# Optimization experiments

Measured on AMD Instinct MI355X. Metric: run time of the kernel, lower is better.

## Reference

```python
import jax, jax.numpy as jnp
import numpy as np

B, S, D, H, L = 2, 4096, 768, 12, 12
DH = D // H
BS = 16                # block size
NB = S // BS           # 256 blocks
NR = 2                 # random blocks per middle query block
DFF = 3072
VOCAB = 50358


def layer_norm(x, s, b):
    m = x.mean(-1, keepdims=True)
    v = ((x - m) ** 2).mean(-1, keepdims=True)
    return (x - m) * jax.lax.rsqrt(v + 1e-12) * s + b


def setup_inputs() -> dict:
    key = jax.random.key(0)
    ks = jax.random.split(key, 20)
    rn = lambda k, shp: jax.random.normal(k, shp, jnp.float32) * 0.02
    # random key-block indices per middle query block, avoiding window+global blocks
    rng = np.random.default_rng(0)
    rb = np.zeros((NB - 2, NR), np.int32)
    for i in range(1, NB - 1):
        forbidden = {0, i - 1, i, i + 1, NB - 1}
        choices = np.array([b for b in range(NB) if b not in forbidden])
        rb[i - 1] = rng.choice(choices, NR, replace=False)
    return {
        "input_ids": jax.random.randint(ks[0], (B, S), 0, VOCAB, jnp.int32),
        "rand_blocks": jnp.asarray(rb),
        "emb_word": rn(ks[1], (VOCAB, D)),
        "emb_pos": rn(ks[2], (S, D)),
        "ln0_s": jnp.ones((D,)), "ln0_b": jnp.zeros((D,)),
        "Wq": rn(ks[3], (L, D, D)), "bq": jnp.zeros((L, D)),
        "Wk": rn(ks[4], (L, D, D)), "bk": jnp.zeros((L, D)),
        "Wv": rn(ks[5], (L, D, D)), "bv": jnp.zeros((L, D)),
        "Wo": rn(ks[6], (L, D, D)), "bo": jnp.zeros((L, D)),
        "ln1_s": jnp.ones((L, D)), "ln1_b": jnp.zeros((L, D)),
        "W1": rn(ks[7], (L, D, DFF)), "b1": jnp.zeros((L, DFF)),
        "W2": rn(ks[8], (L, DFF, D)), "b2": jnp.zeros((L, D)),
        "ln2_s": jnp.ones((L, D)), "ln2_b": jnp.zeros((L, D)),
        "Wp": rn(ks[9], (D, D)), "bp": jnp.zeros((D,)),
        "start_w": jax.random.normal(ks[10], (D,), jnp.float32),
        "end_w": jax.random.normal(ks[11], (D,), jnp.float32),
        "Wd1": rn(ks[12], (D, 20)), "bd1": jnp.zeros((20,)),
        "Wd2": rn(ks[13], (20, 2)), "bd2": jnp.zeros((2,)),
    }


def block_sparse_attn(h, wq, bq_, wk, bk_, wv, bv_, wo, bo_, rand_blocks):
    scale = 1.0 / np.sqrt(DH)
    heads = lambda w, b: (h @ w + b).reshape(B, S, H, DH).transpose(0, 2, 1, 3)
    q = heads(wq, bq_) * scale
    k = heads(wk, bk_)
    v = heads(wv, bv_)
    qb = q.reshape(B, H, NB, BS, DH)
    kb = k.reshape(B, H, NB, BS, DH)
    vb = v.reshape(B, H, NB, BS, DH)
    # global query blocks (first & last) attend to every key
    qg = qb[:, :, jnp.array([0, NB - 1])]                       # [B,H,2,BS,DH]
    ag = jax.nn.softmax(jnp.einsum('bhgqd,bhkd->bhgqk', qg, k), -1)
    og = jnp.einsum('bhgqk,bhkd->bhgqd', ag, v)
    # middle query blocks: global(2) + window(3) + random(2) key blocks
    mid = jnp.arange(1, NB - 1, dtype=jnp.int32)
    idx = jnp.concatenate([
        jnp.zeros((NB - 2, 1), jnp.int32),
        jnp.full((NB - 2, 1), NB - 1, jnp.int32),
        jnp.stack([mid - 1, mid, mid + 1], -1),
        rand_blocks.astype(jnp.int32),
    ], axis=1)                                                  # [NB-2, 7]
    kg = kb[:, :, idx].reshape(B, H, NB - 2, 7 * BS, DH)        # gathered keys
    vg = vb[:, :, idx].reshape(B, H, NB - 2, 7 * BS, DH)
    qm = qb[:, :, 1:NB - 1]                                     # [B,H,NB-2,BS,DH]
    am = jax.nn.softmax(jnp.einsum('bhnqd,bhnkd->bhnqk', qm, kg), -1)
    om = jnp.einsum('bhnqk,bhnkd->bhnqd', am, vg)
    ob = jnp.concatenate([og[:, :, :1], om, og[:, :, 1:]], axis=2)  # [B,H,NB,BS,DH]
    o = ob.reshape(B, H, S, DH).transpose(0, 2, 1, 3).reshape(B, S, D)
    return o @ wo + bo_


def encoder(input_ids, rand_blocks, emb_word, emb_pos, ln0_s, ln0_b,
            Wq, bq, Wk, bk, Wv, bv, Wo, bo, ln1_s, ln1_b,
            W1, b1, W2, b2, ln2_s, ln2_b):
    h = layer_norm(emb_word[input_ids] + emb_pos[None], ln0_s, ln0_b)

    def layer(hc, p):
        wq, bq_, wk, bk_, wv, bv_, wo, bo_, l1s, l1b, w1, b1_, w2, b2_, l2s, l2b = p
        a = block_sparse_attn(hc, wq, bq_, wk, bk_, wv, bv_, wo, bo_, rand_blocks)
        hc = layer_norm(hc + a, l1s, l1b)
        f = jax.nn.gelu(hc @ w1 + b1_, approximate=False) @ w2 + b2_
        hc = layer_norm(hc + f, l2s, l2b)
        return hc, None

    h, _ = jax.lax.scan(layer, h, (Wq, bq, Wk, bk, Wv, bv, Wo, bo,
                                   ln1_s, ln1_b, W1, b1, W2, b2, ln2_s, ln2_b))
    return h


def reference(input_ids, rand_blocks, emb_word, emb_pos, ln0_s, ln0_b,
              Wq, bq, Wk, bk, Wv, bv, Wo, bo, ln1_s, ln1_b,
              W1, b1, W2, b2, ln2_s, ln2_b, Wp, bp,
              start_w, end_w, Wd1, bd1, Wd2, bd2):
    h = encoder(input_ids, rand_blocks, emb_word, emb_pos, ln0_s, ln0_b,
                Wq, bq, Wk, bk, Wv, bv, Wo, bo, ln1_s, ln1_b,
                W1, b1, W2, b2, ln2_s, ln2_b)
    start_logits = h @ start_w        # [B,S]
    end_logits = h @ end_w            # [B,S]
    pooled = jnp.tanh(h[:, 0] @ Wp + bp)   # BERT-style pooler on [CLS]
    d1 = jax.nn.relu(pooled @ Wd1 + bd1)
    disc_logits = d1 @ Wd2 + bd2      # [B,2]
    return start_logits, end_logits, disc_logits
```

## Files before the change

kernel.cpp:

```cpp
#include <hip/hip_runtime.h>

#define DEV __device__ __forceinline__

typedef unsigned short u16;
typedef short bf16x8 __attribute__((ext_vector_type(8)));
typedef float f32x4 __attribute__((ext_vector_type(4)));

constexpr int Bc = 2, Sc = 4096, Dc = 768, Hc = 12, Lc = 12;
constexpr int BSc = 16, NBc = 256, NRc = 2, DFFc = 3072;
constexpr int Mr = Bc * Sc;

DEV u16 f2b(float f) {
  unsigned u = __builtin_bit_cast(unsigned, f);
  u += 0x7fffu + ((u >> 16) & 1u);
  return (u16)(u >> 16);
}
DEV float b2f(u16 u) { return __builtin_bit_cast(float, (unsigned)u << 16); }

DEV void gload_lds16(const void* g, void* l) {
  __builtin_amdgcn_global_load_lds((const __attribute__((address_space(1))) void*)g,
                                   (__attribute__((address_space(3))) void*)l, 16, 0, 0);
}

template<int EPI>
__global__ __launch_bounds__(512, 1)
void gemmP(const u16* __restrict__ A, const u16* __restrict__ Bt,
           const float* __restrict__ bias, u16* __restrict__ Cb,
           u16* __restrict__ Qh, u16* __restrict__ Kh,
           u16* __restrict__ VhT, int M, int N, int K)
{
  __shared__ u16 As[2][128 * 64];
  __shared__ u16 Bs[2][256 * 64];
  const int tid = threadIdx.x;
  const int wid = tid >> 6, lane = tid & 63;
  const int fr = lane & 15, fq = lane >> 4;
  const int wr = wid >> 2, wc = wid & 3;

  int nwg = gridDim.x * gridDim.y;
  int orig = blockIdx.y * gridDim.x + blockIdx.x;
  int swz = (nwg & 7) ? orig : (orig & 7) * (nwg >> 3) + (orig >> 3);
  int bx = swz % gridDim.x, by = swz / gridDim.x;
  const int m0 = by * 128, n0 = bx * 256;

  const u16* asrc[2];
  const u16* bsrc[4];
#pragma unroll
  for (int p = 0; p < 2; ++p) {
    int ci = p * 512 + tid;
    int r = ci >> 3, c = (ci & 7) ^ (r & 7);
    asrc[p] = A + (size_t)(m0 + r) * K + c * 8;
  }
#pragma unroll
  for (int p = 0; p < 4; ++p) {
    int ci = p * 512 + tid;
    int r = ci >> 3, c = (ci & 7) ^ (r & 7);
    bsrc[p] = Bt + (size_t)(n0 + r) * K + c * 8;
  }
  auto stageA = [&](int buf, int k0) {
#pragma unroll
    for (int p = 0; p < 2; ++p)
      gload_lds16(asrc[p] + k0, &As[buf][(p * 512 + tid) * 8]);
  };
  auto stageB = [&](int buf, int k0) {
#pragma unroll
    for (int p = 0; p < 4; ++p)
      gload_lds16(bsrc[p] + k0, &Bs[buf][(p * 512 + tid) * 8]);
  };

  f32x4 acc[4][4] = {};
  const int arow = wr * 64 + fr;
  const int brow = wc * 64 + fr;

  stageA(0, 0);  stageB(0, 0);
  stageA(1, 64); stageB(1, 64);
  asm volatile("s_waitcnt vmcnt(6)" ::: "memory");
  __builtin_amdgcn_sched_barrier(0);
  __builtin_amdgcn_s_barrier();

  const int nt = K >> 6;
  for (int kt = 0; kt < nt; ++kt) {
    const u16* ab = As[kt & 1];
    const u16* bb = Bs[kt & 1];
    bf16x8 aA[2][2], aB[2][2], bA[2][2], bB[2][2];

#pragma unroll
    for (int f = 0; f < 2; ++f)
#pragma unroll
      for (int kh = 0; kh < 2; ++kh) {
        int rowa = arow + f * 16;
        aA[f][kh] = *(const bf16x8*)(ab + rowa * 64 + (((kh * 4 + fq) ^ (rowa & 7)) << 3));
        int rowb = brow + f * 16;
        bA[f][kh] = *(const bf16x8*)(bb + rowb * 64 + (((kh * 4 + fq) ^ (rowb & 7)) << 3));
      }
    __builtin_amdgcn_s_setprio(1);
#pragma unroll
    for (int m = 0; m < 2; ++m)
#pragma unroll
      for (int n = 0; n < 2; ++n)
#pragma unroll
        for (int kh = 0; kh < 2; ++kh)
          acc[m][n] = __builtin_amdgcn_mfma_f32_16x16x32_bf16(aA[m][kh], bA[n][kh], acc[m][n], 0, 0, 0);
    __builtin_amdgcn_s_setprio(0);

#pragma unroll
    for (int f = 0; f < 2; ++f)
#pragma unroll
      for (int kh = 0; kh < 2; ++kh) {
        int rowb = brow + 32 + f * 16;
        bB[f][kh] = *(const bf16x8*)(bb + rowb * 64 + (((kh * 4 + fq) ^ (rowb & 7)) << 3));
      }
    __builtin_amdgcn_s_setprio(1);
#pragma unroll
    for (int m = 0; m < 2; ++m)
#pragma unroll
      for (int n = 0; n < 2; ++n)
#pragma unroll
        for (int kh = 0; kh < 2; ++kh)
          acc[m][n + 2] = __builtin_amdgcn_mfma_f32_16x16x32_bf16(aA[m][kh], bB[n][kh], acc[m][n + 2], 0, 0, 0);
    __builtin_amdgcn_s_setprio(0);
    asm volatile("s_waitcnt lgkmcnt(0)" ::: "memory");
    __builtin_amdgcn_sched_barrier(0);
    __builtin_amdgcn_s_barrier();

    if (kt + 2 < nt) stageB(kt & 1, (kt + 2) * 64);
#pragma unroll
    for (int f = 0; f < 2; ++f)
#pragma unroll
      for (int kh = 0; kh < 2; ++kh) {
        int rowa = arow + 32 + f * 16;
        aB[f][kh] = *(const bf16x8*)(ab + rowa * 64 + (((kh * 4 + fq) ^ (rowa & 7)) << 3));
      }
    __builtin_amdgcn_s_setprio(1);
#pragma unroll
    for (int m = 0; m < 2; ++m)
#pragma unroll
      for (int n = 0; n < 2; ++n)
#pragma unroll
        for (int kh = 0; kh < 2; ++kh)
          acc[m + 2][n] = __builtin_amdgcn_mfma_f32_16x16x32_bf16(aB[m][kh], bA[n][kh], acc[m + 2][n], 0, 0, 0);
    __builtin_amdgcn_s_setprio(0);
    asm volatile("s_waitcnt lgkmcnt(0)" ::: "memory");
    __builtin_amdgcn_sched_barrier(0);
    __builtin_amdgcn_s_barrier();

    if (kt + 2 < nt) stageA(kt & 1, (kt + 2) * 64);
    __builtin_amdgcn_s_setprio(1);
#pragma unroll
    for (int m = 0; m < 2; ++m)
#pragma unroll
      for (int n = 0; n < 2; ++n)
#pragma unroll
        for (int kh = 0; kh < 2; ++kh)
          acc[m + 2][n + 2] = __builtin_amdgcn_mfma_f32_16x16x32_bf16(aB[m][kh], bB[n][kh], acc[m + 2][n + 2], 0, 0, 0);
    __builtin_amdgcn_s_setprio(0);
    if (kt + 1 < nt) {
      if (kt + 2 < nt) asm volatile("s_waitcnt vmcnt(6)" ::: "memory");
      else             asm volatile("s_waitcnt vmcnt(0)" ::: "memory");
      __builtin_amdgcn_sched_barrier(0);
      __builtin_amdgcn_s_barrier();
    }
  }

#pragma unroll
  for (int m = 0; m < 4; ++m) {
#pragma unroll
    for (int n = 0; n < 4; ++n) {
      int col = n0 + wc * 64 + n * 16 + fr;
      float bv = bias[col];
      if constexpr (EPI == 2) {
        int sec = col / 768;
        int c = col - sec * 768;
        int hh = c >> 6, dd = c & 63;
#pragma unroll
        for (int r = 0; r < 4; ++r) {
          int row = m0 + wr * 64 + m * 16 + fq * 4 + r;
          int bb2 = row >> 12, ss = row & 4095;
          size_t bhh = (size_t)(bb2 * Hc + hh);
          u16 val = f2b(acc[m][n][r] + bv);
          if (sec == 0) Qh[(bhh * Sc + ss) * 64 + dd] = val;
          else if (sec == 1) Kh[(bhh * Sc + ss) * 64 + dd] = val;
          else VhT[(bhh * 64 + dd) * Sc + ss] = val;
        }
      } else {
#pragma unroll
        for (int r = 0; r < 4; ++r) {
          int row = m0 + wr * 64 + m * 16 + fq * 4 + r;
          float v = acc[m][n][r] + bv;
          v = 0.5f * v * (1.f + erff(v * 0.70710678118654752f));
          Cb[(size_t)row * N + col] = f2b(v);
        }
      }
    }
  }
}

__global__ __launch_bounds__(256, 2)
void gemmQ(const u16* __restrict__ A, const u16* __restrict__ Bt,
           const float* __restrict__ bias, u16* __restrict__ Cb,
           int M, int N, int K)
{
  __shared__ u16 As[2][128 * 64];
  __shared__ u16 Bs[2][128 * 64];
  const int tid = threadIdx.x;
  const int wid = tid >> 6, lane = tid & 63;
  const int fr = lane & 15, fq = lane >> 4;
  const int wr = wid >> 1, wc = wid & 1;

  int nwg = gridDim.x * gridDim.y;
  int orig = blockIdx.y * gridDim.x + blockIdx.x;
  int swz = (nwg & 7) ? orig : (orig & 7) * (nwg >> 3) + (orig >> 3);
  int bx = swz % gridDim.x, by = swz / gridDim.x;
  const int m0 = by * 128, n0 = bx * 128;

  const u16* asrc[4];
  const u16* bsrc[4];
#pragma unroll
  for (int p = 0; p < 4; ++p) {
    int ci = p * 256 + tid;
    int r = ci >> 3, c = (ci & 7) ^ (r & 7);
    asrc[p] = A + (size_t)(m0 + r) * K + c * 8;
    bsrc[p] = Bt + (size_t)(n0 + r) * K + c * 8;
  }
  auto stageA = [&](int buf, int k0) {
#pragma unroll
    for (int p = 0; p < 4; ++p)
      gload_lds16(asrc[p] + k0, &As[buf][(p * 256 + tid) * 8]);
  };
  auto stageB = [&](int buf, int k0) {
#pragma unroll
    for (int p = 0; p < 4; ++p)
      gload_lds16(bsrc[p] + k0, &Bs[buf][(p * 256 + tid) * 8]);
  };

  f32x4 acc[4][4] = {};
  const int arow = wr * 64 + fr;
  const int brow = wc * 64 + fr;

  stageA(0, 0);  stageB(0, 0);
  stageA(1, 64); stageB(1, 64);
  asm volatile("s_waitcnt vmcnt(8)" ::: "memory");
  __builtin_amdgcn_sched_barrier(0);
  __builtin_amdgcn_s_barrier();

  const int nt = K >> 6;
  for (int kt = 0; kt < nt; ++kt) {
    const u16* ab = As[kt & 1];
    const u16* bb = Bs[kt & 1];
    bf16x8 aA[2][2], aB[2][2], bA[2][2], bB[2][2];

#pragma unroll
    for (int f = 0; f < 2; ++f)
#pragma unroll
      for (int kh = 0; kh < 2; ++kh) {
        int rowa = arow + f * 16;
        aA[f][kh] = *(const bf16x8*)(ab + rowa * 64 + (((kh * 4 + fq) ^ (rowa & 7)) << 3));
        int rowb = brow + f * 16;
        bA[f][kh] = *(const bf16x8*)(bb + rowb * 64 + (((kh * 4 + fq) ^ (rowb & 7)) << 3));
      }
    __builtin_amdgcn_s_setprio(1);
#pragma unroll
    for (int m = 0; m < 2; ++m)
#pragma unroll
      for (int n = 0; n < 2; ++n)
#pragma unroll
        for (int kh = 0; kh < 2; ++kh)
          acc[m][n] = __builtin_amdgcn_mfma_f32_16x16x32_bf16(aA[m][kh], bA[n][kh], acc[m][n], 0, 0, 0);
    __builtin_amdgcn_s_setprio(0);

#pragma unroll
    for (int f = 0; f < 2; ++f)
#pragma unroll
      for (int kh = 0; kh < 2; ++kh) {
        int rowb = brow + 32 + f * 16;
        bB[f][kh] = *(const bf16x8*)(bb + rowb * 64 + (((kh * 4 + fq) ^ (rowb & 7)) << 3));
      }
    __builtin_amdgcn_s_setprio(1);
#pragma unroll
    for (int m = 0; m < 2; ++m)
#pragma unroll
      for (int n = 0; n < 2; ++n)
#pragma unroll
        for (int kh = 0; kh < 2; ++kh)
          acc[m][n + 2] = __builtin_amdgcn_mfma_f32_16x16x32_bf16(aA[m][kh], bB[n][kh], acc[m][n + 2], 0, 0, 0);
    __builtin_amdgcn_s_setprio(0);
    asm volatile("s_waitcnt lgkmcnt(0)" ::: "memory");
    __builtin_amdgcn_sched_barrier(0);
    __builtin_amdgcn_s_barrier();

    if (kt + 2 < nt) stageB(kt & 1, (kt + 2) * 64);
#pragma unroll
    for (int f = 0; f < 2; ++f)
#pragma unroll
      for (int kh = 0; kh < 2; ++kh) {
        int rowa = arow + 32 + f * 16;
        aB[f][kh] = *(const bf16x8*)(ab + rowa * 64 + (((kh * 4 + fq) ^ (rowa & 7)) << 3));
      }
    __builtin_amdgcn_s_setprio(1);
#pragma unroll
    for (int m = 0; m < 2; ++m)
#pragma unroll
      for (int n = 0; n < 2; ++n)
#pragma unroll
        for (int kh = 0; kh < 2; ++kh)
          acc[m + 2][n] = __builtin_amdgcn_mfma_f32_16x16x32_bf16(aB[m][kh], bA[n][kh], acc[m + 2][n], 0, 0, 0);
    __builtin_amdgcn_s_setprio(0);
    asm volatile("s_waitcnt lgkmcnt(0)" ::: "memory");
    __builtin_amdgcn_sched_barrier(0);
    __builtin_amdgcn_s_barrier();

    if (kt + 2 < nt) stageA(kt & 1, (kt + 2) * 64);
    __builtin_amdgcn_s_setprio(1);
#pragma unroll
    for (int m = 0; m < 2; ++m)
#pragma unroll
      for (int n = 0; n < 2; ++n)
#pragma unroll
        for (int kh = 0; kh < 2; ++kh)
          acc[m + 2][n + 2] = __builtin_amdgcn_mfma_f32_16x16x32_bf16(aB[m][kh], bB[n][kh], acc[m + 2][n + 2], 0, 0, 0);
    __builtin_amdgcn_s_setprio(0);
    if (kt + 1 < nt) {
      if (kt + 2 < nt) asm volatile("s_waitcnt vmcnt(8)" ::: "memory");
      else             asm volatile("s_waitcnt vmcnt(0)" ::: "memory");
      __builtin_amdgcn_sched_barrier(0);
      __builtin_amdgcn_s_barrier();
    }
  }

#pragma unroll
  for (int m = 0; m < 4; ++m) {
#pragma unroll
    for (int n = 0; n < 4; ++n) {
      int col = n0 + wc * 64 + n * 16 + fr;
      float bv = bias[col];
#pragma unroll
      for (int r = 0; r < 4; ++r) {
        int row = m0 + wr * 64 + m * 16 + fq * 4 + r;
        Cb[(size_t)row * N + col] = f2b(acc[m][n][r] + bv);
      }
    }
  }
}

__global__ __launch_bounds__(256)
void wtrans_all(const float* __restrict__ Wq, const float* __restrict__ Wk,
                const float* __restrict__ Wv, const float* __restrict__ Wo,
                const float* __restrict__ W1, const float* __restrict__ W2,
                u16* __restrict__ wqkvT, u16* __restrict__ woT,
                u16* __restrict__ w1T, u16* __restrict__ w2T)
{
  int bx = blockIdx.x;
  size_t l = blockIdx.y;
  size_t wsq = l * 768 * 768, wff = l * 768 * 3072;
  const float* in; u16* out; int K, N, ntx, t; float scale = 1.f;
  if (bx < 144)       { in = Wq + wsq; out = wqkvT + l * 2304 * 768;           K = 768;  N = 768;  ntx = 12; t = bx;        scale = 0.125f; }
  else if (bx < 288)  { in = Wk + wsq; out = wqkvT + l * 2304 * 768 + 589824;  K = 768;  N = 768;  ntx = 12; t = bx - 144;  }
  else if (bx < 432)  { in = Wv + wsq; out = wqkvT + l * 2304 * 768 + 1179648; K = 768;  N = 768;  ntx = 12; t = bx - 288;  }
  else if (bx < 576)  { in = Wo + wsq; out = woT + l * 768 * 768;              K = 768;  N = 768;  ntx = 12; t = bx - 432;  }
  else if (bx < 1152) { in = W1 + wff; out = w1T + l * 3072 * 768;             K = 768;  N = 3072; ntx = 48; t = bx - 576;  }
  else                { in = W2 + wff; out = w2T + l * 768 * 3072;             K = 3072; N = 768;  ntx = 12; t = bx - 1152; }
  int n0 = (t % ntx) * 64, k0 = (t / ntx) * 64;
  __shared__ float tl[64][65];
  int tid = threadIdx.x;
  int kr = tid >> 4, nc = (tid & 15) * 4;
#pragma unroll
  for (int kk = 0; kk < 4; ++kk) {
    float4 v = *(const float4*)(in + (size_t)(k0 + kk * 16 + kr) * N + n0 + nc);
    float* d = &tl[kk * 16 + kr][nc];
    d[0] = v.x; d[1] = v.y; d[2] = v.z; d[3] = v.w;
  }
  __syncthreads();
  int k2 = (tid & 31) * 2, nr = tid >> 5;
#pragma unroll
  for (int nn = 0; nn < 8; ++nn) {
    int n = nn * 8 + nr;
    unsigned pk = (unsigned)f2b(tl[k2][n] * scale) | ((unsigned)f2b(tl[k2 + 1][n] * scale) << 16);
    *(unsigned*)(out + (size_t)(n0 + n) * K + k0 + k2) = pk;
  }
}

__global__ void pack_bias(const float* __restrict__ bq, const float* __restrict__ bk,
                          const float* __restrict__ bv, float* __restrict__ bqkv)
{
  int i = blockIdx.x * 256 + threadIdx.x;
  if (i >= Lc * 2304) return;
  int l = i / 2304, j = i % 2304;
  float v = (j < 768) ? bq[(size_t)l * 768 + j] * 0.125f
          : (j < 1536) ? bk[(size_t)l * 768 + j - 768]
                       : bv[(size_t)l * 768 + j - 1536];
  bqkv[i] = v;
}

DEV void breduce2(float& a, float& b) {
  __shared__ float ra[4], rbv[4];
  for (int off = 32; off > 0; off >>= 1) {
    a += __shfl_down(a, off);
    b += __shfl_down(b, off);
  }
  int lane = threadIdx.x & 63, wid = threadIdx.x >> 6;
  if (lane == 0) { ra[wid] = a; rbv[wid] = b; }
  __syncthreads();
  a = ra[0] + ra[1] + ra[2] + ra[3];
  b = rbv[0] + rbv[1] + rbv[2] + rbv[3];
}

__global__ __launch_bounds__(256)
void embed_ln(const int* __restrict__ ids, const float* __restrict__ ew,
              const float* __restrict__ ep, const float* __restrict__ gs,
              const float* __restrict__ gb, float* __restrict__ hout, u16* __restrict__ hb)
{
  int row = blockIdx.x;
  int spos = row & (Sc - 1);
  int id = ids[row];
  int tid = threadIdx.x;
  float x[3], sum = 0.f, ss = 0.f;
#pragma unroll
  for (int j = 0; j < 3; ++j) {
    int i = tid + j * 256;
    x[j] = ew[(size_t)id * Dc + i] + ep[(size_t)spos * Dc + i];
    sum += x[j]; ss += x[j] * x[j];
  }
  breduce2(sum, ss);
  float mean = sum * (1.f / Dc);
  float var = ss * (1.f / Dc) - mean * mean;
  float inv = rsqrtf(var + 1e-12f);
#pragma unroll
  for (int j = 0; j < 3; ++j) {
    int i = tid + j * 256;
    float y = (x[j] - mean) * inv * gs[i] + gb[i];
    hout[(size_t)row * Dc + i] = y;
    hb[(size_t)row * Dc + i] = f2b(y);
  }
}

__global__ __launch_bounds__(256)
void ln_res(const float* __restrict__ X, const u16* __restrict__ Rb,
            const float* __restrict__ gs, const float* __restrict__ gb,
            float* __restrict__ Yf, u16* __restrict__ Yb)
{
  const int wid = threadIdx.x >> 6, lane = threadIdx.x & 63;
  const int row = blockIdx.x * 4 + wid;
  const float* xr = X + (size_t)row * Dc;
  const u16*   rr = Rb + (size_t)row * Dc;
  float x[12];
  float sum = 0.f, ss = 0.f;
#pragma unroll
  for (int p = 0; p < 3; ++p) {
    int c = p * 256 + lane * 4;
    float4 xv = *(const float4*)(xr + c);
    ushort4 rv = *(const ushort4*)(rr + c);
    float v0 = xv.x + b2f(rv.x);
    float v1 = xv.y + b2f(rv.y);
    float v2 = xv.z + b2f(rv.z);
    float v3 = xv.w + b2f(rv.w);
    x[p * 4 + 0] = v0; x[p * 4 + 1] = v1; x[p * 4 + 2] = v2; x[p * 4 + 3] = v3;
    sum += (v0 + v1) + (v2 + v3);
    ss  += (v0 * v0 + v1 * v1) + (v2 * v2 + v3 * v3);
  }
#pragma unroll
  for (int off = 1; off < 64; off <<= 1) {
    sum += __shfl_xor(sum, off);
    ss  += __shfl_xor(ss, off);
  }
  float mean = sum * (1.f / Dc);
  float var = ss * (1.f / Dc) - mean * mean;
  float inv = rsqrtf(var + 1e-12f);
#pragma unroll
  for (int p = 0; p < 3; ++p) {
    int c = p * 256 + lane * 4;
    float4 gv = *(const float4*)(gs + c);
    float4 bv = *(const float4*)(gb + c);
    float y0 = (x[p * 4 + 0] - mean) * inv * gv.x + bv.x;
    float y1 = (x[p * 4 + 1] - mean) * inv * gv.y + bv.y;
    float y2 = (x[p * 4 + 2] - mean) * inv * gv.z + bv.z;
    float y3 = (x[p * 4 + 3] - mean) * inv * gv.w + bv.w;
    float4 yo; yo.x = y0; yo.y = y1; yo.z = y2; yo.w = y3;
    *(float4*)(Yf + (size_t)row * Dc + c) = yo;
    ushort4 pk; pk.x = f2b(y0); pk.y = f2b(y1); pk.z = f2b(y2); pk.w = f2b(y3);
    *(ushort4*)(Yb + (size_t)row * Dc + c) = pk;
  }
}

__global__ __launch_bounds__(256)
void gattn_flash(const u16* __restrict__ Qh, const u16* __restrict__ Kh,
                 const u16* __restrict__ VhT, float* __restrict__ part)
{
  __shared__ u16 pb[4][16 * 136];
  __shared__ float ob[4][16][64];
  __shared__ float mlb[4][2][16];
  const int kc = blockIdx.x, g = blockIdx.y, bh = blockIdx.z;
  const int wid = threadIdx.x >> 6, lane = threadIdx.x & 63;
  const int fr = lane & 15, fq = lane >> 4;
  const int qrow = g ? (NBc - 1) * BSc : 0;

  const u16* Qb = Qh + ((size_t)bh * Sc + qrow) * 64;
  const u16* Kb = Kh + (size_t)bh * Sc * 64;
  const u16* Vt = VhT + (size_t)bh * 64 * Sc;

  bf16x8 qa0 = *(const bf16x8*)(Qb + fr * 64 + fq * 8);
  bf16x8 qa1 = *(const bf16x8*)(Qb + fr * 64 + 32 + fq * 8);

  float m[4], l[4];
  f32x4 o[4] = {};
#pragma unroll
  for (int r = 0; r < 4; ++r) { m[r] = -3.4e38f; l[r] = 0.f; }

  u16* pbw = pb[wid];
  const int s0w = kc * 256 + wid * 64;

  for (int it = 0; it < 2; ++it) {
    const int sb = s0w + it * 32;
    f32x4 s[2];
#pragma unroll
    for (int t = 0; t < 2; ++t) {
      const u16* kr = Kb + (size_t)(sb + t * 16 + fr) * 64 + fq * 8;
      bf16x8 kb0 = *(const bf16x8*)(kr);
      bf16x8 kb1 = *(const bf16x8*)(kr + 32);
      f32x4 a = {};
      a = __builtin_amdgcn_mfma_f32_16x16x32_bf16(qa0, kb0, a, 0, 0, 0);
      a = __builtin_amdgcn_mfma_f32_16x16x32_bf16(qa1, kb1, a, 0, 0, 0);
      s[t] = a;
    }
#pragma unroll
    for (int r = 0; r < 4; ++r) {
      float pm = fmaxf(s[0][r], s[1][r]);
#pragma unroll
      for (int off = 1; off < 16; off <<= 1) pm = fmaxf(pm, __shfl_xor(pm, off));
      float nm = fmaxf(m[r], pm);
      float sc = __expf(m[r] - nm);
      m[r] = nm;
      float e0 = __expf(s[0][r] - nm), e1 = __expf(s[1][r] - nm);
      float ps = e0 + e1;
#pragma unroll
      for (int off = 1; off < 16; off <<= 1) ps += __shfl_xor(ps, off);
      l[r] = l[r] * sc + ps;
#pragma unroll
      for (int nn = 0; nn < 4; ++nn) o[nn][r] *= sc;
      pbw[(fq * 4 + r) * 136 + fr] = f2b(e0);
      pbw[(fq * 4 + r) * 136 + 16 + fr] = f2b(e1);
    }
    asm volatile("s_waitcnt lgkmcnt(0)" ::: "memory");
    __builtin_amdgcn_sched_barrier(0);
    bf16x8 pa = *(const bf16x8*)(pbw + fr * 136 + fq * 8);
#pragma unroll
    for (int nn = 0; nn < 4; ++nn) {
      bf16x8 vb = *(const bf16x8*)(Vt + (size_t)(nn * 16 + fr) * Sc + sb + fq * 8);
      o[nn] = __builtin_amdgcn_mfma_f32_16x16x32_bf16(pa, vb, o[nn], 0, 0, 0);
    }
  }

#pragma unroll
  for (int nn = 0; nn < 4; ++nn)
#pragma unroll
    for (int r = 0; r < 4; ++r)
      ob[wid][fq * 4 + r][nn * 16 + fr] = o[nn][r];
  if (fr == 0) {
#pragma unroll
    for (int r = 0; r < 4; ++r) {
      mlb[wid][0][fq * 4 + r] = m[r];
      mlb[wid][1][fq * 4 + r] = l[r];
    }
  }
  __syncthreads();

  float* pp = part + (size_t)(((bh * 2 + g) * 16) + kc) * 1056;
  int tid = threadIdx.x;
#pragma unroll
  for (int k = 0; k < 4; ++k) {
    int oidx = tid + k * 256;
    int q = oidx >> 6, d = oidx & 63;
    float M = fmaxf(fmaxf(mlb[0][0][q], mlb[1][0][q]), fmaxf(mlb[2][0][q], mlb[3][0][q]));
    float O = 0.f, L = 0.f;
#pragma unroll
    for (int w = 0; w < 4; ++w) {
      float f = __expf(mlb[w][0][q] - M);
      O += f * ob[w][q][d];
      L += f * mlb[w][1][q];
    }
    pp[q * 64 + d] = O;
    if (d == 0) { pp[1024 + q] = M; pp[1040 + q] = L; }
  }
}

__global__ __launch_bounds__(256)
void attn_tail(const u16* __restrict__ Qh, const u16* __restrict__ Kh,
               const u16* __restrict__ VhT, const int* __restrict__ rb,
               const float* __restrict__ part, u16* __restrict__ attnb)
{
  if (blockIdx.x < 48) {
    int idx = blockIdx.x;
    int bh = idx >> 1, g = idx & 1;
    int b = bh / Hc, h = bh % Hc;
    int tid = threadIdx.x;
    const float* pbase = part + (size_t)idx * 16 * 1056;
#pragma unroll
    for (int k = 0; k < 4; ++k) {
      int oidx = tid + k * 256;
      int q = oidx >> 6, d = oidx & 63;
      float M = -3.4e38f;
#pragma unroll
      for (int c = 0; c < 16; ++c) M = fmaxf(M, pbase[c * 1056 + 1024 + q]);
      float O = 0.f, L = 0.f;
#pragma unroll
      for (int c = 0; c < 16; ++c) {
        float f = __expf(pbase[c * 1056 + 1024 + q] - M);
        O += f * pbase[c * 1056 + q * 64 + d];
        L += f * pbase[c * 1056 + 1040 + q];
      }
      int srow = (g ? (NBc - 1) * BSc : 0) + q;
      attnb[((size_t)(b * Sc + srow)) * Dc + h * 64 + d] = f2b(O / L);
    }
    return;
  }

  __shared__ u16 pb[4][16 * 136];
  const int wid = threadIdx.x >> 6, lane = threadIdx.x & 63;
  const int w = (blockIdx.x - 48) * 4 + wid;
  const int n = w % 254, bh = w / 254;
  const int b = bh / Hc, h = bh % Hc;
  const int fr = lane & 15, fq = lane >> 4;

  int idx[7];
  idx[0] = 0; idx[1] = NBc - 1; idx[2] = n; idx[3] = n + 1; idx[4] = n + 2;
  idx[5] = rb[n * NRc]; idx[6] = rb[n * NRc + 1];

  const u16* Qb = Qh + ((size_t)bh * Sc + (n + 1) * BSc) * 64;
  const u16* Kb = Kh + (size_t)bh * Sc * 64;
  const u16* Vt = VhT + (size_t)bh * 64 * Sc;

  bf16x8 qa0 = *(const bf16x8*)(Qb + fr * 64 + fq * 8);
  bf16x8 qa1 = *(const bf16x8*)(Qb + fr * 64 + 32 + fq * 8);

  f32x4 s[7];
#pragma unroll
  for (int t = 0; t < 7; ++t) {
    const u16* kr = Kb + ((size_t)idx[t] * BSc + fr) * 64 + fq * 8;
    bf16x8 kb0 = *(const bf16x8*)(kr);
    bf16x8 kb1 = *(const bf16x8*)(kr + 32);
    f32x4 a = {};
    a = __builtin_amdgcn_mfma_f32_16x16x32_bf16(qa0, kb0, a, 0, 0, 0);
    a = __builtin_amdgcn_mfma_f32_16x16x32_bf16(qa1, kb1, a, 0, 0, 0);
    s[t] = a;
  }

  float mx[4], sm[4];
#pragma unroll
  for (int r = 0; r < 4; ++r) {
    mx[r] = s[0][r];
#pragma unroll
    for (int t = 1; t < 7; ++t) mx[r] = fmaxf(mx[r], s[t][r]);
  }
#pragma unroll
  for (int off = 1; off < 16; off <<= 1)
#pragma unroll
    for (int r = 0; r < 4; ++r) mx[r] = fmaxf(mx[r], __shfl_xor(mx[r], off));
#pragma unroll
  for (int r = 0; r < 4; ++r) sm[r] = 0.f;
#pragma unroll
  for (int t = 0; t < 7; ++t)
#pragma unroll
    for (int r = 0; r < 4; ++r) { float e = expf(s[t][r] - mx[r]); s[t][r] = e; sm[r] += e; }
#pragma unroll
  for (int off = 1; off < 16; off <<= 1)
#pragma unroll
    for (int r = 0; r < 4; ++r) sm[r] += __shfl_xor(sm[r], off);
  float inv[4];
#pragma unroll
  for (int r = 0; r < 4; ++r) inv[r] = 1.f / sm[r];

  u16* pbw = pb[wid];
#pragma unroll
  for (int t = 0; t < 7; ++t)
#pragma unroll
    for (int r = 0; r < 4; ++r)
      pbw[(fq * 4 + r) * 136 + t * 16 + fr] = f2b(s[t][r] * inv[r]);
  for (int i = lane; i < 16 * 24; i += 64) {
    int rr = i / 24, cc = 112 + i % 24;
    pbw[rr * 136 + cc] = 0;
  }
  __syncthreads();

  f32x4 o[4] = {};
#pragma unroll
  for (int ks = 0; ks < 4; ++ks) {
    bf16x8 pa = *(const bf16x8*)(pbw + fr * 136 + ks * 32 + fq * 8);
    int t = ks * 2 + (fq >> 1);
    int tt = (t < 7) ? t : 0;
    size_t voff = (size_t)idx[tt] * BSc + (fq & 1) * 8;
#pragma unroll
    for (int nn = 0; nn < 4; ++nn) {
      bf16x8 vb = *(const bf16x8*)(Vt + (size_t)(nn * 16 + fr) * Sc + voff);
      o[nn] = __builtin_amdgcn_mfma_f32_16x16x32_bf16(pa, vb, o[nn], 0, 0, 0);
    }
  }

  size_t rbase = (size_t)b * Sc + (n + 1) * BSc;
#pragma unroll
  for (int nn = 0; nn < 4; ++nn)
#pragma unroll
    for (int r = 0; r < 4; ++r)
      attnb[(rbase + fq * 4 + r) * Dc + h * 64 + nn * 16 + fr] = f2b(o[nn][r]);
}

__global__ __launch_bounds__(256)
void logits_k(const float* __restrict__ h, const float* __restrict__ sw,
              const float* __restrict__ ew, float* __restrict__ out)
{
  int row = blockIdx.x;
  int tid = threadIdx.x;
  float s1 = 0.f, s2 = 0.f;
#pragma unroll
  for (int j = 0; j < 3; ++j) {
    int i = tid + j * 256;
    float x = h[(size_t)row * Dc + i];
    s1 += x * sw[i]; s2 += x * ew[i];
  }
  breduce2(s1, s2);
  if (tid == 0) { out[row] = s1; out[Mr + row] = s2; }
}

__global__ __launch_bounds__(256)
void pooled_k(const float* __restrict__ h, const float* __restrict__ Wp,
              const float* __restrict__ bp, float* __restrict__ pooled)
{
  int b = blockIdx.y, j0 = blockIdx.x * 64;
  int jl = threadIdx.x & 63, kp = threadIdx.x >> 6;
  __shared__ float hr[768];
  __shared__ float part[4][64];
  for (int i = threadIdx.x; i < 768; i += 256) hr[i] = h[(size_t)b * Sc * Dc + i];
  __syncthreads();
  float a0 = 0.f, a1 = 0.f, a2 = 0.f, a3 = 0.f;
  const float* wp = Wp + (size_t)(kp * 192) * 768 + j0 + jl;
  const float* hk = hr + kp * 192;
#pragma unroll 4
  for (int k = 0; k < 192; k += 4) {
    a0 += hk[k]     * wp[(size_t)k * 768];
    a1 += hk[k + 1] * wp[(size_t)(k + 1) * 768];
    a2 += hk[k + 2] * wp[(size_t)(k + 2) * 768];
    a3 += hk[k + 3] * wp[(size_t)(k + 3) * 768];
  }
  part[kp][jl] = a0 + a1 + a2 + a3;
  __syncthreads();
  if (threadIdx.x < 64) {
    float s = part[0][jl] + part[1][jl] + part[2][jl] + part[3][jl] + bp[j0 + jl];
    pooled[b * 768 + j0 + jl] = tanhf(s);
  }
}

__global__ __launch_bounds__(256)
void head2(const float* __restrict__ pooled, const float* __restrict__ Wd1,
           const float* __restrict__ bd1, const float* __restrict__ Wd2,
           const float* __restrict__ bd2, float* __restrict__ out)
{
  __shared__ float pl[1536];
  __shared__ float part[40][6];
  __shared__ float d1[40];
  int tid = threadIdx.x;
  for (int i = tid; i < 1536; i += 256) pl[i] = pooled[i];
  __syncthreads();
  if (tid < 240) {
    int p = tid / 6, s = tid % 6;
    int b = p / 20, u = p % 20;
    float a = 0.f;
    for (int k = s * 128; k < s * 128 + 128; ++k) a += pl[b * 768 + k] * Wd1[(size_t)k * 20 + u];
    part[p][s] = a;
  }
  __syncthreads();
  if (tid < 40) {
    float a = bd1[tid % 20];
#pragma unroll
    for (int s = 0; s < 6; ++s) a += part[tid][s];
    d1[tid] = fmaxf(a, 0.f);
  }
  __syncthreads();
  if (tid < 4) {
    int b = tid >> 1, o = tid & 1;
    float a = bd2[o];
#pragma unroll
    for (int k = 0; k < 20; ++k) a += d1[b * 20 + k] * Wd2[k * 2 + o];
    out[2 * Mr + b * 2 + o] = a;
  }
}

extern "C" void kernel_launch(void* const* d_in, const int* in_sizes, int n_in,
                              void* d_out, int out_size, void* d_ws, size_t ws_size,
                              hipStream_t stream)
{
  (void)in_sizes; (void)n_in; (void)out_size; (void)ws_size;
  const int*   ids   = (const int*)d_in[0];
  const int*   rbp   = (const int*)d_in[1];
  const float* emb_w = (const float*)d_in[2];
  const float* emb_p = (const float*)d_in[3];
  const float* ln0s  = (const float*)d_in[4];
  const float* ln0b  = (const float*)d_in[5];
  const float* Wq    = (const float*)d_in[6];
  const float* bq    = (const float*)d_in[7];
  const float* Wk    = (const float*)d_in[8];
  const float* bk    = (const float*)d_in[9];
  const float* Wv    = (const float*)d_in[10];
  const float* bv    = (const float*)d_in[11];
  const float* Wo    = (const float*)d_in[12];
  const float* bo    = (const float*)d_in[13];
  const float* ln1s  = (const float*)d_in[14];
  const float* ln1b  = (const float*)d_in[15];
  const float* W1    = (const float*)d_in[16];
  const float* b1    = (const float*)d_in[17];
  const float* W2    = (const float*)d_in[18];
  const float* b2    = (const float*)d_in[19];
  const float* ln2s  = (const float*)d_in[20];
  const float* ln2b  = (const float*)d_in[21];
  const float* Wp    = (const float*)d_in[22];
  const float* bp    = (const float*)d_in[23];
  const float* sw    = (const float*)d_in[24];
  const float* ewv   = (const float*)d_in[25];
  const float* Wd1   = (const float*)d_in[26];
  const float* bd1   = (const float*)d_in[27];
  const float* Wd2   = (const float*)d_in[28];
  const float* bd2   = (const float*)d_in[29];
  float* out = (float*)d_out;

  unsigned char* pc = (unsigned char*)d_ws;
  auto carve = [&](size_t bytes) {
    void* r = (void*)pc;
    pc += (bytes + 255) & ~(size_t)255;
    return r;
  };
  u16*   wqkvT = (u16*)carve((size_t)Lc * 2304 * 768 * 2);
  u16*   woT   = (u16*)carve((size_t)Lc * 768 * 768 * 2);
  u16*   w1T   = (u16*)carve((size_t)Lc * 3072 * 768 * 2);
  u16*   w2T   = (u16*)carve((size_t)Lc * 768 * 3072 * 2);
  float* bqkv  = (float*)carve((size_t)Lc * 2304 * 4);
  float* h     = (float*)carve((size_t)Mr * Dc * 4);
  u16*   hb    = (u16*)carve((size_t)Mr * Dc * 2);
  u16*   Qh    = (u16*)carve((size_t)Mr * Dc * 2);
  u16*   Kh    = (u16*)carve((size_t)Mr * Dc * 2);
  u16*   VhT   = (u16*)carve((size_t)Mr * Dc * 2);
  u16*   attnb = (u16*)carve((size_t)Mr * Dc * 2);
  u16*   c0b   = (u16*)carve((size_t)Mr * Dc * 2);
  float* pool2 = (float*)carve((size_t)Bc * Dc * 4);
  float* m1ws  = (float*)carve((size_t)Mr * DFFc * 2);
  u16*   m1    = (u16*)m1ws;
  float* part  = (float*)((unsigned char*)m1ws + (size_t)13 * 1024 * 1024);

  pack_bias<<<(Lc * 2304 + 255) / 256, 256, 0, stream>>>(bq, bk, bv, bqkv);
  wtrans_all<<<dim3(1728, Lc), 256, 0, stream>>>(Wq, Wk, Wv, Wo, W1, W2,
                                                 wqkvT, woT, w1T, w2T);
  embed_ln<<<Mr, 256, 0, stream>>>(ids, emb_w, emb_p, ln0s, ln0b, h, hb);

  for (int l = 0; l < Lc; ++l) {
    gemmP<2><<<dim3(9, 64), 512, 0, stream>>>(hb, wqkvT + (size_t)l * 2304 * 768,
                                              bqkv + (size_t)l * 2304,
                                              nullptr, Qh, Kh, VhT, Mr, 2304, 768);
    gattn_flash<<<dim3(16, 2, Bc * Hc), 256, 0, stream>>>(Qh, Kh, VhT, part);
    attn_tail<<<48 + 1524, 256, 0, stream>>>(Qh, Kh, VhT, rbp, part, attnb);
    gemmQ<<<dim3(6, 64), 256, 0, stream>>>(attnb, woT + (size_t)l * 768 * 768,
                                           bo + (size_t)l * 768, c0b, Mr, 768, 768);
    ln_res<<<Mr / 4, 256, 0, stream>>>(h, c0b, ln1s + (size_t)l * 768, ln1b + (size_t)l * 768, h, hb);
    gemmP<1><<<dim3(12, 64), 512, 0, stream>>>(hb, w1T + (size_t)l * 3072 * 768,
                                               b1 + (size_t)l * 3072,
                                               m1, nullptr, nullptr, nullptr,
                                               Mr, 3072, 768);
    gemmQ<<<dim3(6, 64), 256, 0, stream>>>(m1, w2T + (size_t)l * 768 * 3072,
                                           b2 + (size_t)l * 768, c0b, Mr, 768, 3072);
    ln_res<<<Mr / 4, 256, 0, stream>>>(h, c0b, ln2s + (size_t)l * 768, ln2b + (size_t)l * 768, h, hb);
  }

  logits_k<<<Mr, 256, 0, stream>>>(h, sw, ewv, out);
  pooled_k<<<dim3(12, Bc), 256, 0, stream>>>(h, Wp, bp, pool2);
  head2<<<1, 256, 0, stream>>>(pool2, Wd1, bd1, Wd2, bd2, out);
}
```

Measured before the change: 3.582 ms.

## Merge global flash attention with middle-block attention, split out small reduce

Global-query flash partial blocks and sliding/random middle-block attention now run in one launch, and the global partial reduction moves into a small separate kernel. This lets the 768 global blocks overlap with the 1524 middle blocks instead of serialising two launches, leaving only a tiny 48-block reduce afterwards. Separately, the weight-transpose kernel writes 16-byte packed stores instead of 4-byte stores. Launch count is unchanged, and the reduce kernel adds a small serial tail.

```diff
diff --git a/kernel.cpp b/kernel.cpp
--- a/kernel.cpp
+++ b/kernel.cpp
@@ -369,12 +369,16 @@
     d[0] = v.x; d[1] = v.y; d[2] = v.z; d[3] = v.w;
   }
   __syncthreads();
-  int k2 = (tid & 31) * 2, nr = tid >> 5;
-#pragma unroll
-  for (int nn = 0; nn < 8; ++nn) {
-    int n = nn * 8 + nr;
-    unsigned pk = (unsigned)f2b(tl[k2][n] * scale) | ((unsigned)f2b(tl[k2 + 1][n] * scale) << 16);
-    *(unsigned*)(out + (size_t)(n0 + n) * K + k0 + k2) = pk;
+  int k8 = (tid & 7) * 8, nb = tid >> 3;
+#pragma unroll
+  for (int half = 0; half < 2; ++half) {
+    int n = nb + half * 32;
+    unsigned pk0 = (unsigned)f2b(tl[k8 + 0][n] * scale) | ((unsigned)f2b(tl[k8 + 1][n] * scale) << 16);
+    unsigned pk1 = (unsigned)f2b(tl[k8 + 2][n] * scale) | ((unsigned)f2b(tl[k8 + 3][n] * scale) << 16);
+    unsigned pk2 = (unsigned)f2b(tl[k8 + 4][n] * scale) | ((unsigned)f2b(tl[k8 + 5][n] * scale) << 16);
+    unsigned pk3 = (unsigned)f2b(tl[k8 + 6][n] * scale) | ((unsigned)f2b(tl[k8 + 7][n] * scale) << 16);
+    uint4 pk; pk.x = pk0; pk.y = pk1; pk.z = pk2; pk.w = pk3;
+    *(uint4*)(out + (size_t)(n0 + n) * K + k0 + k8) = pk;
   }
 }
 
@@ -481,143 +485,114 @@
 }
 
 __global__ __launch_bounds__(256)
-void gattn_flash(const u16* __restrict__ Qh, const u16* __restrict__ Kh,
-                 const u16* __restrict__ VhT, float* __restrict__ part)
+void gattn_fm(const u16* __restrict__ Qh, const u16* __restrict__ Kh,
+              const u16* __restrict__ VhT, const int* __restrict__ rb,
+              float* __restrict__ part, u16* __restrict__ attnb)
 {
   __shared__ u16 pb[4][16 * 136];
   __shared__ float ob[4][16][64];
   __shared__ float mlb[4][2][16];
-  const int kc = blockIdx.x, g = blockIdx.y, bh = blockIdx.z;
   const int wid = threadIdx.x >> 6, lane = threadIdx.x & 63;
   const int fr = lane & 15, fq = lane >> 4;
-  const int qrow = g ? (NBc - 1) * BSc : 0;
-
-  const u16* Qb = Qh + ((size_t)bh * Sc + qrow) * 64;
-  const u16* Kb = Kh + (size_t)bh * Sc * 64;
-  const u16* Vt = VhT + (size_t)bh * 64 * Sc;
-
-  bf16x8 qa0 = *(const bf16x8*)(Qb + fr * 64 + fq * 8);
-  bf16x8 qa1 = *(const bf16x8*)(Qb + fr * 64 + 32 + fq * 8);
-
-  float m[4], l[4];
-  f32x4 o[4] = {};
-#pragma unroll
-  for (int r = 0; r < 4; ++r) { m[r] = -3.4e38f; l[r] = 0.f; }
-
-  u16* pbw = pb[wid];
-  const int s0w = kc * 256 + wid * 64;
-
-  for (int it = 0; it < 2; ++it) {
-    const int sb = s0w + it * 32;
-    f32x4 s[2];
-#pragma unroll
-    for (int t = 0; t < 2; ++t) {
-      const u16* kr = Kb + (size_t)(sb + t * 16 + fr) * 64 + fq * 8;
-      bf16x8 kb0 = *(const bf16x8*)(kr);
-      bf16x8 kb1 = *(const bf16x8*)(kr + 32);
-      f32x4 a = {};
-      a = __builtin_amdgcn_mfma_f32_16x16x32_bf16(qa0, kb0, a, 0, 0, 0);
-      a = __builtin_amdgcn_mfma_f32_16x16x32_bf16(qa1, kb1, a, 0, 0, 0);
-      s[t] = a;
+  const int bxg = blockIdx.x;
+
+  if (bxg < 768) {
+    const int kc = bxg & 15, g = (bxg >> 4) & 1, bh = bxg >> 5;
+    const int qrow = g ? (NBc - 1) * BSc : 0;
+
+    const u16* Qb = Qh + ((size_t)bh * Sc + qrow) * 64;
+    const u16* Kb = Kh + (size_t)bh * Sc * 64;
+    const u16* Vt = VhT + (size_t)bh * 64 * Sc;
+
+    bf16x8 qa0 = *(const bf16x8*)(Qb + fr * 64 + fq * 8);
+    bf16x8 qa1 = *(const bf16x8*)(Qb + fr * 64 + 32 + fq * 8);
+
+    float m[4], l[4];
+    f32x4 o[4] = {};
+#pragma unroll
+    for (int r = 0; r < 4; ++r) { m[r] = -3.4e38f; l[r] = 0.f; }
+
+    u16* pbw = pb[wid];
+    const int s0w = kc * 256 + wid * 64;
+
+    for (int it = 0; it < 2; ++it) {
+      const int sb = s0w + it * 32;
+      f32x4 s[2];
+#pragma unroll
+      for (int t = 0; t < 2; ++t) {
+        const u16* kr = Kb + (size_t)(sb + t * 16 + fr) * 64 + fq * 8;
+        bf16x8 kb0 = *(const bf16x8*)(kr);
+        bf16x8 kb1 = *(const bf16x8*)(kr + 32);
+        f32x4 a = {};
+        a = __builtin_amdgcn_mfma_f32_16x16x32_bf16(qa0, kb0, a, 0, 0, 0);
+        a = __builtin_amdgcn_mfma_f32_16x16x32_bf16(qa1, kb1, a, 0, 0, 0);
+        s[t] = a;
+      }
+#pragma unroll
+      for (int r = 0; r < 4; ++r) {
+        float pm = fmaxf(s[0][r], s[1][r]);
+#pragma unroll
+        for (int off = 1; off < 16; off <<= 1) pm = fmaxf(pm, __shfl_xor(pm, off));
+        float nm = fmaxf(m[r], pm);
+        float sc = __expf(m[r] - nm);
+        m[r] = nm;
+        float e0 = __expf(s[0][r] - nm), e1 = __expf(s[1][r] - nm);
+        float ps = e0 + e1;
+#pragma unroll
+        for (int off = 1; off < 16; off <<= 1) ps += __shfl_xor(ps, off);
+        l[r] = l[r] * sc + ps;
+#pragma unroll
+        for (int nn = 0; nn < 4; ++nn) o[nn][r] *= sc;
+        pbw[(fq * 4 + r) * 136 + fr] = f2b(e0);
+        pbw[(fq * 4 + r) * 136 + 16 + fr] = f2b(e1);
+      }
+      asm volatile("s_waitcnt lgkmcnt(0)" ::: "memory");
+      __builtin_amdgcn_sched_barrier(0);
+      bf16x8 pa = *(const bf16x8*)(pbw + fr * 136 + fq * 8);
+#pragma unroll
+      for (int nn = 0; nn < 4; ++nn) {
+        bf16x8 vb = *(const bf16x8*)(Vt + (size_t)(nn * 16 + fr) * Sc + sb + fq * 8);
+        o[nn] = __builtin_amdgcn_mfma_f32_16x16x32_bf16(pa, vb, o[nn], 0, 0, 0);
+      }
     }
-#pragma unroll
-    for (int r = 0; r < 4; ++r) {
-      float pm = fmaxf(s[0][r], s[1][r]);
-#pragma unroll
-      for (int off = 1; off < 16; off <<= 1) pm = fmaxf(pm, __shfl_xor(pm, off));
-      float nm = fmaxf(m[r], pm);
-      float sc = __expf(m[r] - nm);
-      m[r] = nm;
-      float e0 = __expf(s[0][r] - nm), e1 = __expf(s[1][r] - nm);
-      float ps = e0 + e1;
-#pragma unroll
-      for (int off = 1; off < 16; off <<= 1) ps += __shfl_xor(ps, off);
-      l[r] = l[r] * sc + ps;
-#pragma unroll
-      for (int nn = 0; nn < 4; ++nn) o[nn][r] *= sc;
-      pbw[(fq * 4 + r) * 136 + fr] = f2b(e0);
-      pbw[(fq * 4 + r) * 136 + 16 + fr] = f2b(e1);
+
+#pragma unroll
+    for (int nn = 0; nn < 4; ++nn)
+#pragma unroll
+      for (int r = 0; r < 4; ++r)
+        ob[wid][fq * 4 + r][nn * 16 + fr] = o[nn][r];
+    if (fr == 0) {
+#pragma unroll
+      for (int r = 0; r < 4; ++r) {
+        mlb[wid][0][fq * 4 + r] = m[r];
+        mlb[wid][1][fq * 4 + r] = l[r];
+      }
     }
-    asm volatile("s_waitcnt lgkmcnt(0)" ::: "memory");
-    __builtin_amdgcn_sched_barrier(0);
-    bf16x8 pa = *(const bf16x8*)(pbw + fr * 136 + fq * 8);
-#pragma unroll
-    for (int nn = 0; nn < 4; ++nn) {
-      bf16x8 vb = *(const bf16x8*)(Vt + (size_t)(nn * 16 + fr) * Sc + sb + fq * 8);
-      o[nn] = __builtin_amdgcn_mfma_f32_16x16x32_bf16(pa, vb, o[nn], 0, 0, 0);
-    }
-  }
-
-#pragma unroll
-  for (int nn = 0; nn < 4; ++nn)
-#pragma unroll
-    for (int r = 0; r < 4; ++r)
-      ob[wid][fq * 4 + r][nn * 16 + fr] = o[nn][r];
-  if (fr == 0) {
-#pragma unroll
-    for (int r = 0; r < 4; ++r) {
-      mlb[wid][0][fq * 4 + r] = m[r];
-      mlb[wid][1][fq * 4 + r] = l[r];
-    }
-  }
-  __syncthreads();
-
-  float* pp = part + (size_t)(((bh * 2 + g) * 16) + kc) * 1056;
-  int tid = threadIdx.x;
-#pragma unroll
-  for (int k = 0; k < 4; ++k) {
-    int oidx = tid + k * 256;
-    int q = oidx >> 6, d = oidx & 63;
-    float M = fmaxf(fmaxf(mlb[0][0][q], mlb[1][0][q]), fmaxf(mlb[2][0][q], mlb[3][0][q]));
-    float O = 0.f, L = 0.f;
-#pragma unroll
-    for (int w = 0; w < 4; ++w) {
-      float f = __expf(mlb[w][0][q] - M);
-      O += f * ob[w][q][d];
-      L += f * mlb[w][1][q];
-    }
-    pp[q * 64 + d] = O;
-    if (d == 0) { pp[1024 + q] = M; pp[1040 + q] = L; }
-  }
-}
-
-__global__ __launch_bounds__(256)
-void attn_tail(const u16* __restrict__ Qh, const u16* __restrict__ Kh,
-               const u16* __restrict__ VhT, const int* __restrict__ rb,
-               const float* __restrict__ part, u16* __restrict__ attnb)
-{
-  if (blockIdx.x < 48) {
-    int idx = blockIdx.x;
-    int bh = idx >> 1, g = idx & 1;
-    int b = bh / Hc, h = bh % Hc;
+    __syncthreads();
+
+    float* pp = part + (size_t)(((bh * 2 + g) * 16) + kc) * 1056;
     int tid = threadIdx.x;
-    const float* pbase = part + (size_t)idx * 16 * 1056;
 #pragma unroll
     for (int k = 0; k < 4; ++k) {
       int oidx = tid + k * 256;
       int q = oidx >> 6, d = oidx & 63;
-      float M = -3.4e38f;
-#pragma unroll
-      for (int c = 0; c < 16; ++c) M = fmaxf(M, pbase[c * 1056 + 1024 + q]);
+      float M = fmaxf(fmaxf(mlb[0][0][q], mlb[1][0][q]), fmaxf(mlb[2][0][q], mlb[3][0][q]));
       float O = 0.f, L = 0.f;
 #pragma unroll
-      for (int c = 0; c < 16; ++c) {
-        float f = __expf(pbase[c * 1056 + 1024 + q] - M);
-        O += f * pbase[c * 1056 + q * 64 + d];
-        L += f * pbase[c * 1056 + 1040 + q];
-      }
-      int srow = (g ? (NBc - 1) * BSc : 0) + q;
-      attnb[((size_t)(b * Sc + srow)) * Dc + h * 64 + d] = f2b(O / L);
+      for (int w = 0; w < 4; ++w) {
+        float f = __expf(mlb[w][0][q] - M);
+        O += f * ob[w][q][d];
+        L += f * mlb[w][1][q];
+      }
+      pp[q * 64 + d] = O;
+      if (d == 0) { pp[1024 + q] = M; pp[1040 + q] = L; }
     }
     return;
   }
 
-  __shared__ u16 pb[4][16 * 136];
-  const int wid = threadIdx.x >> 6, lane = threadIdx.x & 63;
-  const int w = (blockIdx.x - 48) * 4 + wid;
+  const int w = (bxg - 768) * 4 + wid;
   const int n = w % 254, bh = w / 254;
   const int b = bh / Hc, h = bh % Hc;
-  const int fr = lane & 15, fq = lane >> 4;
 
   int idx[7];
   idx[0] = 0; idx[1] = NBc - 1; idx[2] = n; idx[3] = n + 1; idx[4] = n + 2;
@@ -699,6 +674,33 @@
 #pragma unroll
     for (int r = 0; r < 4; ++r)
       attnb[(rbase + fq * 4 + r) * Dc + h * 64 + nn * 16 + fr] = f2b(o[nn][r]);
+}
+
+__global__ __launch_bounds__(256)
+void gattn_reduce(const float* __restrict__ part, u16* __restrict__ attnb)
+{
+  int idx = blockIdx.x;
+  int bh = idx >> 1, g = idx & 1;
+  int b = bh / Hc, h = bh % Hc;
+  int tid = threadIdx.x;
+  const float* pbase = part + (size_t)idx * 16 * 1056;
+#pragma unroll
+  for (int k = 0; k < 4; ++k) {
+    int oidx = tid + k * 256;
+    int q = oidx >> 6, d = oidx & 63;
+    float M = -3.4e38f;
+#pragma unroll
+    for (int c = 0; c < 16; ++c) M = fmaxf(M, pbase[c * 1056 + 1024 + q]);
+    float O = 0.f, L = 0.f;
+#pragma unroll
+    for (int c = 0; c < 16; ++c) {
+      float f = __expf(pbase[c * 1056 + 1024 + q] - M);
+      O += f * pbase[c * 1056 + q * 64 + d];
+      L += f * pbase[c * 1056 + 1040 + q];
+    }
+    int srow = (g ? (NBc - 1) * BSc : 0) + q;
+    attnb[((size_t)(b * Sc + srow)) * Dc + h * 64 + d] = f2b(O / L);
+  }
 }
 
 __global__ __launch_bounds__(256)
@@ -850,8 +852,8 @@
     gemmP<2><<<dim3(9, 64), 512, 0, stream>>>(hb, wqkvT + (size_t)l * 2304 * 768,
                                               bqkv + (size_t)l * 2304,
                                               nullptr, Qh, Kh, VhT, Mr, 2304, 768);
-    gattn_flash<<<dim3(16, 2, Bc * Hc), 256, 0, stream>>>(Qh, Kh, VhT, part);
-    attn_tail<<<48 + 1524, 256, 0, stream>>>(Qh, Kh, VhT, rbp, part, attnb);
+    gattn_fm<<<768 + 1524, 256, 0, stream>>>(Qh, Kh, VhT, rbp, part, attnb);
+    gattn_reduce<<<48, 256, 0, stream>>>(part, attnb);
     gemmQ<<<dim3(6, 64), 256, 0, stream>>>(attnb, woT + (size_t)l * 768 * 768,
                                            bo + (size_t)l * 768, c0b, Mr, 768, 768);
     ln_res<<<Mr / 4, 256, 0, stream>>>(h, c0b, ln1s + (size_t)l * 768, ln1b + (size_t)l * 768, h, hb);
```

Measured after the change: 3.617 ms. About the same (+1.0%).
